# Kernel tuning notes

Hardware: AMD Instinct MI355X
Metric: run time of the kernel (lower is better)

Reference implementation:

```python
import jax, jax.numpy as jnp
import numpy as np

N_PARTS = 4
HIDDEN = 256
NUM_FREQS = 10
IN_DIM = 3
EMB_DIM = IN_DIM * (1 + 2 * NUM_FREQS)  # 63
PART_DIM = HIDDEN // N_PARTS


def _embed(x):
    freqs = 2.0 ** jnp.arange(NUM_FREQS, dtype=x.dtype)        # [F]
    xf = x[..., None, :] * freqs[:, None]                      # [..., F, 3]
    enc = jnp.stack([jnp.sin(xf), jnp.cos(xf)], axis=-2)       # [..., F, 2, 3]
    enc = enc.reshape(x.shape[:-1] + (NUM_FREQS * 2 * IN_DIM,))
    return jnp.concatenate([x, enc], axis=-1)                  # [..., 63]


def _masks():
    # contiguous 0/1 per-part neuron masks over the HIDDEN axis (ClassMaskCreator)
    m = np.zeros((N_PARTS, HIDDEN), dtype=np.float32)
    for p in range(N_PARTS):
        s = p * PART_DIM
        e = HIDDEN if p == N_PARTS - 1 else s + PART_DIM
        m[p, s:e] = 1.0
    return jnp.asarray(m)


def setup_inputs() -> dict:
    key = jax.random.key(0)
    ks = jax.random.split(key, 8)
    B, N = 1, 131072

    def lin(k, fan_in, fan_out):
        return jax.random.normal(k, (fan_in, fan_out), jnp.float32) / np.float32(np.sqrt(fan_in))

    return {
        "coords": jax.random.normal(ks[0], (B, N, IN_DIM), jnp.float32),
        "W0": lin(ks[1], EMB_DIM, HIDDEN), "b0": jnp.zeros((HIDDEN,), jnp.float32),
        "W1": lin(ks[2], HIDDEN, HIDDEN), "b1": jnp.zeros((HIDDEN,), jnp.float32),
        "W2": lin(ks[3], HIDDEN, HIDDEN), "b2": jnp.zeros((HIDDEN,), jnp.float32),
        "Wocc": lin(ks[4], HIDDEN, 1), "bocc": jnp.zeros((1,), jnp.float32),
        "Wc": jax.random.normal(ks[5], (N_PARTS, HIDDEN), jnp.float32) / np.float32(np.sqrt(HIDDEN)),
        "bc": jnp.zeros((N_PARTS,), jnp.float32),
    }


def reference(coords, W0, b0, W1, b1, W2, b2, Wocc, bocc, Wc, bc):
    masks = _masks()                                  # [P, H]
    x = _embed(coords) @ W0 + b0                      # [B, N, H]  (no activation after layer 0, per source)

    # occupancy trunk: relu(L1) -> relu(L2) -> occ head
    x_occ = jax.nn.relu(x @ W1 + b1)
    x_occ = jax.nn.relu(x_occ @ W2 + b2)
    occ = x_occ @ Wocc + bocc                         # [B, N, 1]

    # part branches. Loop iteration i=0 masks x; i=1 indexes temporal_part_output[1*part_id],
    # i.e. the i=0 outputs. The i=1 outputs (h2) are dead w.r.t. all returned values because
    # part_features[part_id] for part_id in 0..P-1 selects the first P (i=0) entries.
    h1 = [jax.nn.relu((x * masks[p]) @ W1 + b1) for p in range(N_PARTS)]  # [B, N, H] each

    # class heads: class_heads[p](h1[p] * mask_p).squeeze(0), concatenated on last dim
    cls = [jnp.squeeze((h1[p] * masks[p]) @ Wc[p][:, None] + bc[p], axis=0)
           for p in range(N_PARTS)]                   # [N, 1] each (B == 1)
    part_class = jnp.concatenate(cls, axis=-1)        # [N, P]

    return occ, part_class
```

## Files before the change

kernel.cpp:

```cpp
#include <hip/hip_runtime.h>


#define NPTS 131072
#define M_PB 64
#define AST 264

typedef _Float16 half8   __attribute__((ext_vector_type(8)));
typedef _Float16 half4_t __attribute__((ext_vector_type(4)));
typedef __fp16   fp16x2  __attribute__((ext_vector_type(2)));
typedef float    float4_t __attribute__((ext_vector_type(4)));

__global__ void prep(const float* __restrict__ W0, const float* __restrict__ W1,
                     const float* __restrict__ W2, _Float16* __restrict__ ws) {
  int id = blockIdx.x * 256 + threadIdx.x;
  _Float16 v;
  if (id < 16384) {
    int e = id, j = e & 7, l = (e >> 3) & 63, kb = (e >> 9) & 1, tt = e >> 10;
    int c = l & 15, q = l >> 4;
    int k = kb * 32 + q * 8 + j, n = tt * 16 + c;
    v = (k < 63) ? (_Float16)W0[k * 256 + n] : (_Float16)0.f;
  } else if (id < 81920) {
    int e = id - 16384, j = e & 7, l = (e >> 3) & 63, kb = (e >> 9) & 7, tt = e >> 12;
    int c = l & 15, q = l >> 4;
    int k = kb * 32 + q * 8 + j, n = tt * 16 + c;
    v = (_Float16)W1[k * 256 + n];
  } else {
    int e = id - 81920, j = e & 7, l = (e >> 3) & 63, kb = (e >> 9) & 7, tt = e >> 12;
    int c = l & 15, q = l >> 4;
    int k = kb * 32 + q * 8 + j, n = tt * 16 + c;
    v = (_Float16)W2[k * 256 + n];
  }
  ws[id] = v;
}

__device__ __forceinline__ half4_t pack4(float a, float b, float cc, float d) {
  fp16x2 p0 = __builtin_amdgcn_cvt_pkrtz(a, b);
  fp16x2 p1 = __builtin_amdgcn_cvt_pkrtz(cc, d);
  half4_t h;
  h[0] = (_Float16)p0[0]; h[1] = (_Float16)p0[1];
  h[2] = (_Float16)p1[0]; h[3] = (_Float16)p1[1];
  return h;
}

__global__ __launch_bounds__(256, 3) void mlp_main(
    const float* __restrict__ coords,
    const _Float16* __restrict__ W0sw,
    const _Float16* __restrict__ W1sw,
    const _Float16* __restrict__ W2sw,
    const float* __restrict__ b0, const float* __restrict__ b1,
    const float* __restrict__ b2,
    const float* __restrict__ Wocc, const float* __restrict__ bocc,
    const float* __restrict__ Wc, const float* __restrict__ bc,
    float* __restrict__ out) {
  __shared__ _Float16 actX[M_PB * AST];
  __shared__ float occ_s[4][M_PB];

  const int t = threadIdx.x;
  const int w = t >> 6;
  const int l = t & 63;
  const int c = l & 15;
  const int q = l >> 4;
  const int m0 = blockIdx.x * M_PB;

  {
    const float* cp = coords + (size_t)(m0 + l) * 3;
    float x0 = cp[0], x1 = cp[1], x2 = cp[2];
    float v[16];
#pragma unroll
    for (int u = 0; u < 16; ++u) {
      int k = 16 * w + u;
      float r;
      if (k >= 63) r = 0.f;
      else if (k < 3) r = (k == 0) ? x0 : (k == 1 ? x1 : x2);
      else {
        int kk = k - 3;
        int f = kk / 6;
        int rem = kk - 6 * f;
        int s = (rem >= 3) ? 1 : 0;
        int i3 = rem - 3 * s;
        float xi = (i3 == 0) ? x0 : (i3 == 1 ? x1 : x2);
        float arg = xi * (float)(1 << f);
        float nn = rintf(arg * 0.15915494309189535f);
        float rr = fmaf(nn, -6.28318548202514648f, arg);
        rr = fmaf(nn, 1.7484555e-7f, rr);
        r = s ? __cosf(rr) : __sinf(rr);
      }
      v[u] = r;
    }
    half8 e0, e1;
#pragma unroll
    for (int u = 0; u < 4; ++u) {
      fp16x2 p = __builtin_amdgcn_cvt_pkrtz(v[2 * u], v[2 * u + 1]);
      e0[2 * u] = (_Float16)p[0]; e0[2 * u + 1] = (_Float16)p[1];
      fp16x2 p2 = __builtin_amdgcn_cvt_pkrtz(v[8 + 2 * u], v[9 + 2 * u]);
      e1[2 * u] = (_Float16)p2[0]; e1[2 * u + 1] = (_Float16)p2[1];
    }
    *(half8*)&actX[l * AST + 16 * w] = e0;
    *(half8*)&actX[l * AST + 16 * w + 8] = e1;
  }
  __syncthreads();

  float4_t acc[4][4];
  const _Float16* ap = actX + c * AST + q * 8;

  {
    const _Float16* wb = W0sw + (size_t)(w * 4) * 1024 + l * 8;
    half8 a0[4], a1[4];
#pragma unroll
    for (int tn = 0; tn < 4; ++tn) {
      a0[tn] = *(const half8*)(wb + tn * 1024);
      a1[tn] = *(const half8*)(wb + tn * 1024 + 512);
    }
#pragma unroll
    for (int tn = 0; tn < 4; ++tn) {
      float4_t bz = *(const float4_t*)(b0 + 64 * w + tn * 16 + q * 4);
#pragma unroll
      for (int tm = 0; tm < 4; ++tm) acc[tn][tm] = bz;
    }
#pragma unroll
    for (int kb = 0; kb < 2; ++kb) {
      half8 b[4];
#pragma unroll
      for (int tm = 0; tm < 4; ++tm) b[tm] = *(const half8*)(ap + tm * 16 * AST + kb * 32);
#pragma unroll
      for (int tn = 0; tn < 4; ++tn)
#pragma unroll
        for (int tm = 0; tm < 4; ++tm)
          acc[tn][tm] = __builtin_amdgcn_mfma_f32_16x16x32_f16(
              kb ? a1[tn] : a0[tn], b[tm], acc[tn][tm], 0, 0, 0);
    }
  }
  __syncthreads();
#pragma unroll
  for (int tn = 0; tn < 4; ++tn)
#pragma unroll
    for (int tm = 0; tm < 4; ++tm) {
      float4_t v = acc[tn][tm];
      *(half4_t*)&actX[(tm * 16 + c) * AST + 64 * w + tn * 16 + q * 4] =
          pack4(v[0], v[1], v[2], v[3]);
    }
  __syncthreads();

  {
    const _Float16* wb = W1sw + (size_t)(w * 4) * 4096 + l * 8;
    const int w2 = 2 * w;
    float bcw = bc[w];
#pragma unroll
    for (int tn = 0; tn < 4; ++tn) {
      float4_t bz = *(const float4_t*)(b1 + 64 * w + tn * 16 + q * 4);
#pragma unroll
      for (int tm = 0; tm < 4; ++tm) acc[tn][tm] = bz;
    }
    auto kbof = [&](int j) {
      return (j < 2) ? (w2 + j) : ((j - 2) + ((j - 2) >= w2 ? 2 : 0));
    };
    half8 a[4], an[4];
#pragma unroll
    for (int tn = 0; tn < 4; ++tn) a[tn] = *(const half8*)(wb + tn * 4096 + kbof(0) * 512);
#pragma unroll
    for (int j = 0; j < 8; ++j) {
      const int kb = kbof(j);
      half8 b[4];
#pragma unroll
      for (int tm = 0; tm < 4; ++tm) b[tm] = *(const half8*)(ap + tm * 16 * AST + kb * 32);
      if (j + 1 < 8) {
        const int kbn = kbof(j + 1);
#pragma unroll
        for (int tn = 0; tn < 4; ++tn) an[tn] = *(const half8*)(wb + tn * 4096 + kbn * 512);
      }
#pragma unroll
      for (int tn = 0; tn < 4; ++tn)
#pragma unroll
        for (int tm = 0; tm < 4; ++tm)
          acc[tn][tm] = __builtin_amdgcn_mfma_f32_16x16x32_f16(a[tn], b[tm], acc[tn][tm], 0, 0, 0);
      if (j == 1) {
        float pcls[4] = {0.f, 0.f, 0.f, 0.f};
#pragma unroll
        for (int tn = 0; tn < 4; ++tn) {
          float4_t wcv = *(const float4_t*)(Wc + 256 * w + 64 * w + tn * 16 + q * 4);
#pragma unroll
          for (int tm = 0; tm < 4; ++tm) {
            float4_t v = acc[tn][tm];
#pragma unroll
            for (int r = 0; r < 4; ++r) pcls[tm] += fmaxf(v[r], 0.f) * wcv[r];
          }
        }
#pragma unroll
        for (int tm = 0; tm < 4; ++tm) {
          float s = pcls[tm];
          s += __shfl_xor(s, 16, 64);
          s += __shfl_xor(s, 32, 64);
          if (l < 16)
            out[(size_t)NPTS + (size_t)(m0 + tm * 16 + c) * 4 + w] = s + bcw;
        }
      }
      if (j + 1 < 8) {
#pragma unroll
        for (int tn = 0; tn < 4; ++tn) a[tn] = an[tn];
      }
    }
  }
  __syncthreads();
#pragma unroll
  for (int tn = 0; tn < 4; ++tn)
#pragma unroll
    for (int tm = 0; tm < 4; ++tm) {
      float4_t v = acc[tn][tm];
      *(half4_t*)&actX[(tm * 16 + c) * AST + 64 * w + tn * 16 + q * 4] =
          pack4(fmaxf(v[0], 0.f), fmaxf(v[1], 0.f), fmaxf(v[2], 0.f), fmaxf(v[3], 0.f));
    }
  __syncthreads();

  {
    const _Float16* wb = W2sw + (size_t)(w * 4) * 4096 + l * 8;
#pragma unroll
    for (int tn = 0; tn < 4; ++tn) {
      float4_t bz = *(const float4_t*)(b2 + 64 * w + tn * 16 + q * 4);
#pragma unroll
      for (int tm = 0; tm < 4; ++tm) acc[tn][tm] = bz;
    }
    half8 a[4], an[4];
#pragma unroll
    for (int tn = 0; tn < 4; ++tn) a[tn] = *(const half8*)(wb + tn * 4096);
#pragma unroll
    for (int kb = 0; kb < 8; ++kb) {
      half8 b[4];
#pragma unroll
      for (int tm = 0; tm < 4; ++tm) b[tm] = *(const half8*)(ap + tm * 16 * AST + kb * 32);
      if (kb + 1 < 8) {
#pragma unroll
        for (int tn = 0; tn < 4; ++tn)
          an[tn] = *(const half8*)(wb + tn * 4096 + (kb + 1) * 512);
      }
#pragma unroll
      for (int tn = 0; tn < 4; ++tn)
#pragma unroll
        for (int tm = 0; tm < 4; ++tm)
          acc[tn][tm] = __builtin_amdgcn_mfma_f32_16x16x32_f16(a[tn], b[tm], acc[tn][tm], 0, 0, 0);
      if (kb + 1 < 8) {
#pragma unroll
        for (int tn = 0; tn < 4; ++tn) a[tn] = an[tn];
      }
    }
    float pocc[4] = {0.f, 0.f, 0.f, 0.f};
#pragma unroll
    for (int tn = 0; tn < 4; ++tn) {
      float4_t wov = *(const float4_t*)(Wocc + 64 * w + tn * 16 + q * 4);
#pragma unroll
      for (int tm = 0; tm < 4; ++tm) {
        float4_t v = acc[tn][tm];
#pragma unroll
        for (int r = 0; r < 4; ++r) pocc[tm] += fmaxf(v[r], 0.f) * wov[r];
      }
    }
#pragma unroll
    for (int tm = 0; tm < 4; ++tm) {
      float s = pocc[tm];
      s += __shfl_xor(s, 16, 64);
      s += __shfl_xor(s, 32, 64);
      if (l < 16) occ_s[w][tm * 16 + c] = s;
    }
  }
  __syncthreads();
  if (t < M_PB) {
    out[m0 + t] = occ_s[0][t] + occ_s[1][t] + occ_s[2][t] + occ_s[3][t] + bocc[0];
  }
}

extern "C" void kernel_launch(void* const* d_in, const int* in_sizes, int n_in,
                              void* d_out, int out_size, void* d_ws, size_t ws_size,
                              hipStream_t stream) {
  const float* coords = (const float*)d_in[0];
  const float* W0   = (const float*)d_in[1];
  const float* b0   = (const float*)d_in[2];
  const float* W1   = (const float*)d_in[3];
  const float* b1   = (const float*)d_in[4];
  const float* W2   = (const float*)d_in[5];
  const float* b2   = (const float*)d_in[6];
  const float* Wocc = (const float*)d_in[7];
  const float* bocc = (const float*)d_in[8];
  const float* Wc   = (const float*)d_in[9];
  const float* bc   = (const float*)d_in[10];
  float* out = (float*)d_out;

  _Float16* ws = (_Float16*)d_ws;
  _Float16* W0sw = ws;
  _Float16* W1sw = ws + 16384;
  _Float16* W2sw = ws + 81920;

  prep<<<576, 256, 0, stream>>>(W0, W1, W2, ws);
  mlp_main<<<NPTS / M_PB, 256, 0, stream>>>(coords, W0sw, W1sw, W2sw,
                                            b0, b1, b2, Wocc, bocc, Wc, bc, out);
}
```

Before: 121.9 us.

## Double per-block point tile to 128 and deepen weight prefetch to three stages

Each block now handles 128 points instead of 64, so every wave runs a 4x8 grid of MFMA tiles and reuses each weight fragment across twice as many points, roughly halving weight traffic per point. The swizzled weight layout is reordered so that each wave's 64-column slice is contiguous per k-block. The one-stage weight prefetch becomes a rotating three-stage register buffer. The cost is double the accumulator registers and larger LDS use, with launch bounds lowered to 2 blocks per SM, so occupancy falls and register spills are possible.

```diff
diff --git a/kernel.cpp b/kernel.cpp
--- a/kernel.cpp
+++ b/kernel.cpp
@@ -2,7 +2,7 @@
 
 
 #define NPTS 131072
-#define M_PB 64
+#define M_PB 128
 #define AST 264
 
 typedef _Float16 half8   __attribute__((ext_vector_type(8)));
@@ -15,19 +15,16 @@
   int id = blockIdx.x * 256 + threadIdx.x;
   _Float16 v;
   if (id < 16384) {
-    int e = id, j = e & 7, l = (e >> 3) & 63, kb = (e >> 9) & 1, tt = e >> 10;
-    int c = l & 15, q = l >> 4;
-    int k = kb * 32 + q * 8 + j, n = tt * 16 + c;
+    int e = id, j = e & 7, l = (e >> 3) & 63, tn = (e >> 9) & 3, kb = (e >> 11) & 1, s = e >> 12;
+    int k = kb * 32 + (l >> 4) * 8 + j, n = s * 64 + tn * 16 + (l & 15);
     v = (k < 63) ? (_Float16)W0[k * 256 + n] : (_Float16)0.f;
   } else if (id < 81920) {
-    int e = id - 16384, j = e & 7, l = (e >> 3) & 63, kb = (e >> 9) & 7, tt = e >> 12;
-    int c = l & 15, q = l >> 4;
-    int k = kb * 32 + q * 8 + j, n = tt * 16 + c;
+    int e = id - 16384, j = e & 7, l = (e >> 3) & 63, tn = (e >> 9) & 3, kb = (e >> 11) & 7, s = e >> 14;
+    int k = kb * 32 + (l >> 4) * 8 + j, n = s * 64 + tn * 16 + (l & 15);
     v = (_Float16)W1[k * 256 + n];
   } else {
-    int e = id - 81920, j = e & 7, l = (e >> 3) & 63, kb = (e >> 9) & 7, tt = e >> 12;
-    int c = l & 15, q = l >> 4;
-    int k = kb * 32 + q * 8 + j, n = tt * 16 + c;
+    int e = id - 81920, j = e & 7, l = (e >> 3) & 63, tn = (e >> 9) & 3, kb = (e >> 11) & 7, s = e >> 14;
+    int k = kb * 32 + (l >> 4) * 8 + j, n = s * 64 + tn * 16 + (l & 15);
     v = (_Float16)W2[k * 256 + n];
   }
   ws[id] = v;
@@ -42,7 +39,7 @@
   return h;
 }
 
-__global__ __launch_bounds__(256, 3) void mlp_main(
+__global__ __launch_bounds__(256, 2) void mlp_main(
     const float* __restrict__ coords,
     const _Float16* __restrict__ W0sw,
     const _Float16* __restrict__ W1sw,
@@ -63,69 +60,70 @@
   const int m0 = blockIdx.x * M_PB;
 
   {
-    const float* cp = coords + (size_t)(m0 + l) * 3;
+    int m = t & 127, kh = (t >> 7) * 32;
+    const float* cp = coords + (size_t)(m0 + m) * 3;
     float x0 = cp[0], x1 = cp[1], x2 = cp[2];
-    float v[16];
-#pragma unroll
-    for (int u = 0; u < 16; ++u) {
-      int k = 16 * w + u;
-      float r;
-      if (k >= 63) r = 0.f;
-      else if (k < 3) r = (k == 0) ? x0 : (k == 1 ? x1 : x2);
-      else {
-        int kk = k - 3;
-        int f = kk / 6;
-        int rem = kk - 6 * f;
-        int s = (rem >= 3) ? 1 : 0;
-        int i3 = rem - 3 * s;
-        float xi = (i3 == 0) ? x0 : (i3 == 1 ? x1 : x2);
-        float arg = xi * (float)(1 << f);
-        float nn = rintf(arg * 0.15915494309189535f);
-        float rr = fmaf(nn, -6.28318548202514648f, arg);
-        rr = fmaf(nn, 1.7484555e-7f, rr);
-        r = s ? __cosf(rr) : __sinf(rr);
-      }
-      v[u] = r;
-    }
-    half8 e0, e1;
-#pragma unroll
-    for (int u = 0; u < 4; ++u) {
-      fp16x2 p = __builtin_amdgcn_cvt_pkrtz(v[2 * u], v[2 * u + 1]);
-      e0[2 * u] = (_Float16)p[0]; e0[2 * u + 1] = (_Float16)p[1];
-      fp16x2 p2 = __builtin_amdgcn_cvt_pkrtz(v[8 + 2 * u], v[9 + 2 * u]);
-      e1[2 * u] = (_Float16)p2[0]; e1[2 * u + 1] = (_Float16)p2[1];
-    }
-    *(half8*)&actX[l * AST + 16 * w] = e0;
-    *(half8*)&actX[l * AST + 16 * w + 8] = e1;
-  }
-  __syncthreads();
-
-  float4_t acc[4][4];
+#pragma unroll
+    for (int i = 0; i < 4; ++i) {
+      float v[8];
+#pragma unroll
+      for (int u = 0; u < 8; ++u) {
+        int k = kh + i * 8 + u;
+        float r;
+        if (k >= 63) r = 0.f;
+        else if (k < 3) r = (k == 0) ? x0 : (k == 1 ? x1 : x2);
+        else {
+          int kk = k - 3;
+          int f = kk / 6;
+          int rem = kk - 6 * f;
+          int s = (rem >= 3) ? 1 : 0;
+          int i3 = rem - 3 * s;
+          float xi = (i3 == 0) ? x0 : (i3 == 1 ? x1 : x2);
+          float arg = xi * (float)(1 << f);
+          float nn = rintf(arg * 0.15915494309189535f);
+          float rr = fmaf(nn, -6.28318548202514648f, arg);
+          rr = fmaf(nn, 1.7484555e-7f, rr);
+          r = s ? __cosf(rr) : __sinf(rr);
+        }
+        v[u] = r;
+      }
+      half8 ev;
+#pragma unroll
+      for (int u = 0; u < 4; ++u) {
+        fp16x2 p = __builtin_amdgcn_cvt_pkrtz(v[2 * u], v[2 * u + 1]);
+        ev[2 * u] = (_Float16)p[0]; ev[2 * u + 1] = (_Float16)p[1];
+      }
+      *(half8*)&actX[m * AST + kh + i * 8] = ev;
+    }
+  }
+  __syncthreads();
+
+  float4_t acc[4][8];
   const _Float16* ap = actX + c * AST + q * 8;
 
   {
-    const _Float16* wb = W0sw + (size_t)(w * 4) * 1024 + l * 8;
+    const _Float16* wb = W0sw + (size_t)w * 4096 + l * 8;
     half8 a0[4], a1[4];
 #pragma unroll
     for (int tn = 0; tn < 4; ++tn) {
-      a0[tn] = *(const half8*)(wb + tn * 1024);
-      a1[tn] = *(const half8*)(wb + tn * 1024 + 512);
+      a0[tn] = *(const half8*)(wb + tn * 512);
+      a1[tn] = *(const half8*)(wb + 2048 + tn * 512);
     }
 #pragma unroll
     for (int tn = 0; tn < 4; ++tn) {
       float4_t bz = *(const float4_t*)(b0 + 64 * w + tn * 16 + q * 4);
 #pragma unroll
-      for (int tm = 0; tm < 4; ++tm) acc[tn][tm] = bz;
+      for (int tm = 0; tm < 8; ++tm) acc[tn][tm] = bz;
     }
 #pragma unroll
     for (int kb = 0; kb < 2; ++kb) {
-      half8 b[4];
-#pragma unroll
-      for (int tm = 0; tm < 4; ++tm) b[tm] = *(const half8*)(ap + tm * 16 * AST + kb * 32);
-#pragma unroll
-      for (int tn = 0; tn < 4; ++tn)
-#pragma unroll
-        for (int tm = 0; tm < 4; ++tm)
+      half8 b[8];
+#pragma unroll
+      for (int tm = 0; tm < 8; ++tm) b[tm] = *(const half8*)(ap + tm * 16 * AST + kb * 32);
+#pragma unroll
+      for (int tn = 0; tn < 4; ++tn)
+#pragma unroll
+        for (int tm = 0; tm < 8; ++tm)
           acc[tn][tm] = __builtin_amdgcn_mfma_f32_16x16x32_f16(
               kb ? a1[tn] : a0[tn], b[tm], acc[tn][tm], 0, 0, 0);
     }
@@ -134,7 +132,7 @@
 #pragma unroll
   for (int tn = 0; tn < 4; ++tn)
 #pragma unroll
-    for (int tm = 0; tm < 4; ++tm) {
+    for (int tm = 0; tm < 8; ++tm) {
       float4_t v = acc[tn][tm];
       *(half4_t*)&actX[(tm * 16 + c) * AST + 64 * w + tn * 16 + q * 4] =
           pack4(v[0], v[1], v[2], v[3]);
@@ -142,51 +140,51 @@
   __syncthreads();
 
   {
-    const _Float16* wb = W1sw + (size_t)(w * 4) * 4096 + l * 8;
+    const _Float16* wb = W1sw + (size_t)w * 16384 + l * 8;
     const int w2 = 2 * w;
     float bcw = bc[w];
 #pragma unroll
     for (int tn = 0; tn < 4; ++tn) {
       float4_t bz = *(const float4_t*)(b1 + 64 * w + tn * 16 + q * 4);
 #pragma unroll
-      for (int tm = 0; tm < 4; ++tm) acc[tn][tm] = bz;
+      for (int tm = 0; tm < 8; ++tm) acc[tn][tm] = bz;
     }
     auto kbof = [&](int j) {
       return (j < 2) ? (w2 + j) : ((j - 2) + ((j - 2) >= w2 ? 2 : 0));
     };
-    half8 a[4], an[4];
-#pragma unroll
-    for (int tn = 0; tn < 4; ++tn) a[tn] = *(const half8*)(wb + tn * 4096 + kbof(0) * 512);
+    half8 A[3][4];
+#pragma unroll
+    for (int p = 0; p < 3; ++p) {
+      const _Float16* pa = wb + kbof(p) * 2048;
+#pragma unroll
+      for (int tn = 0; tn < 4; ++tn) A[p][tn] = *(const half8*)(pa + tn * 512);
+    }
 #pragma unroll
     for (int j = 0; j < 8; ++j) {
       const int kb = kbof(j);
-      half8 b[4];
-#pragma unroll
-      for (int tm = 0; tm < 4; ++tm) b[tm] = *(const half8*)(ap + tm * 16 * AST + kb * 32);
-      if (j + 1 < 8) {
-        const int kbn = kbof(j + 1);
-#pragma unroll
-        for (int tn = 0; tn < 4; ++tn) an[tn] = *(const half8*)(wb + tn * 4096 + kbn * 512);
-      }
-#pragma unroll
-      for (int tn = 0; tn < 4; ++tn)
-#pragma unroll
-        for (int tm = 0; tm < 4; ++tm)
-          acc[tn][tm] = __builtin_amdgcn_mfma_f32_16x16x32_f16(a[tn], b[tm], acc[tn][tm], 0, 0, 0);
+      half8 b[8];
+#pragma unroll
+      for (int tm = 0; tm < 8; ++tm) b[tm] = *(const half8*)(ap + tm * 16 * AST + kb * 32);
+#pragma unroll
+      for (int tn = 0; tn < 4; ++tn)
+#pragma unroll
+        for (int tm = 0; tm < 8; ++tm)
+          acc[tn][tm] = __builtin_amdgcn_mfma_f32_16x16x32_f16(
+              A[j % 3][tn], b[tm], acc[tn][tm], 0, 0, 0);
       if (j == 1) {
-        float pcls[4] = {0.f, 0.f, 0.f, 0.f};
+        float pcls[8] = {0.f, 0.f, 0.f, 0.f, 0.f, 0.f, 0.f, 0.f};
 #pragma unroll
         for (int tn = 0; tn < 4; ++tn) {
           float4_t wcv = *(const float4_t*)(Wc + 256 * w + 64 * w + tn * 16 + q * 4);
 #pragma unroll
-          for (int tm = 0; tm < 4; ++tm) {
+          for (int tm = 0; tm < 8; ++tm) {
             float4_t v = acc[tn][tm];
 #pragma unroll
             for (int r = 0; r < 4; ++r) pcls[tm] += fmaxf(v[r], 0.f) * wcv[r];
           }
         }
 #pragma unroll
-        for (int tm = 0; tm < 4; ++tm) {
+        for (int tm = 0; tm < 8; ++tm) {
           float s = pcls[tm];
           s += __shfl_xor(s, 16, 64);
           s += __shfl_xor(s, 32, 64);
@@ -194,9 +192,10 @@
             out[(size_t)NPTS + (size_t)(m0 + tm * 16 + c) * 4 + w] = s + bcw;
         }
       }
-      if (j + 1 < 8) {
-#pragma unroll
-        for (int tn = 0; tn < 4; ++tn) a[tn] = an[tn];
+      if (j + 3 < 8) {
+        const _Float16* pa = wb + kbof(j + 3) * 2048;
+#pragma unroll
+        for (int tn = 0; tn < 4; ++tn) A[j % 3][tn] = *(const half8*)(pa + tn * 512);
       }
     }
   }
@@ -204,7 +203,7 @@
 #pragma unroll
   for (int tn = 0; tn < 4; ++tn)
 #pragma unroll
-    for (int tm = 0; tm < 4; ++tm) {
+    for (int tm = 0; tm < 8; ++tm) {
       float4_t v = acc[tn][tm];
       *(half4_t*)&actX[(tm * 16 + c) * AST + 64 * w + tn * 16 + q * 4] =
           pack4(fmaxf(v[0], 0.f), fmaxf(v[1], 0.f), fmaxf(v[2], 0.f), fmaxf(v[3], 0.f));
@@ -212,49 +211,49 @@
   __syncthreads();
 
   {
-    const _Float16* wb = W2sw + (size_t)(w * 4) * 4096 + l * 8;
+    const _Float16* wb = W2sw + (size_t)w * 16384 + l * 8;
 #pragma unroll
     for (int tn = 0; tn < 4; ++tn) {
       float4_t bz = *(const float4_t*)(b2 + 64 * w + tn * 16 + q * 4);
 #pragma unroll
-      for (int tm = 0; tm < 4; ++tm) acc[tn][tm] = bz;
-    }
-    half8 a[4], an[4];
-#pragma unroll
-    for (int tn = 0; tn < 4; ++tn) a[tn] = *(const half8*)(wb + tn * 4096);
+      for (int tm = 0; tm < 8; ++tm) acc[tn][tm] = bz;
+    }
+    half8 A[3][4];
+#pragma unroll
+    for (int p = 0; p < 3; ++p)
+#pragma unroll
+      for (int tn = 0; tn < 4; ++tn)
+        A[p][tn] = *(const half8*)(wb + p * 2048 + tn * 512);
 #pragma unroll
     for (int kb = 0; kb < 8; ++kb) {
-      half8 b[4];
-#pragma unroll
-      for (int tm = 0; tm < 4; ++tm) b[tm] = *(const half8*)(ap + tm * 16 * AST + kb * 32);
-      if (kb + 1 < 8) {
+      half8 b[8];
+#pragma unroll
+      for (int tm = 0; tm < 8; ++tm) b[tm] = *(const half8*)(ap + tm * 16 * AST + kb * 32);
+#pragma unroll
+      for (int tn = 0; tn < 4; ++tn)
+#pragma unroll
+        for (int tm = 0; tm < 8; ++tm)
+          acc[tn][tm] = __builtin_amdgcn_mfma_f32_16x16x32_f16(
+              A[kb % 3][tn], b[tm], acc[tn][tm], 0, 0, 0);
+      if (kb + 3 < 8) {
 #pragma unroll
         for (int tn = 0; tn < 4; ++tn)
-          an[tn] = *(const half8*)(wb + tn * 4096 + (kb + 1) * 512);
-      }
-#pragma unroll
-      for (int tn = 0; tn < 4; ++tn)
-#pragma unroll
-        for (int tm = 0; tm < 4; ++tm)
-          acc[tn][tm] = __builtin_amdgcn_mfma_f32_16x16x32_f16(a[tn], b[tm], acc[tn][tm], 0, 0, 0);
-      if (kb + 1 < 8) {
-#pragma unroll
-        for (int tn = 0; tn < 4; ++tn) a[tn] = an[tn];
-      }
-    }
-    float pocc[4] = {0.f, 0.f, 0.f, 0.f};
+          A[kb % 3][tn] = *(const half8*)(wb + (kb + 3) * 2048 + tn * 512);
+      }
+    }
+    float pocc[8] = {0.f, 0.f, 0.f, 0.f, 0.f, 0.f, 0.f, 0.f};
 #pragma unroll
     for (int tn = 0; tn < 4; ++tn) {
       float4_t wov = *(const float4_t*)(Wocc + 64 * w + tn * 16 + q * 4);
 #pragma unroll
-      for (int tm = 0; tm < 4; ++tm) {
+      for (int tm = 0; tm < 8; ++tm) {
         float4_t v = acc[tn][tm];
 #pragma unroll
         for (int r = 0; r < 4; ++r) pocc[tm] += fmaxf(v[r], 0.f) * wov[r];
       }
     }
 #pragma unroll
-    for (int tm = 0; tm < 4; ++tm) {
+    for (int tm = 0; tm < 8; ++tm) {
       float s = pocc[tm];
       s += __shfl_xor(s, 16, 64);
       s += __shfl_xor(s, 32, 64);
```

Result: faster. 115.6 us (-5.1%).

## Reorder swizzled weights per wave and double-buffer global weight prefetch across layers

Applied to the files above, without the earlier changes.

Changes the prep swizzle so each wave's weight fragments for a k-block sit contiguously, and writes the embedding into a separate small LDS buffer so layer-0 no longer needs a barrier before reusing actX. Weight fragments are now prefetched two k-blocks ahead and across layer boundaries (next layer's first fragments load while the current epilogue runs), and LDS activation reads are software-pipelined one step ahead. The aim is to hide global-memory weight latency and remove one syncthreads, at the cost of more registers and extra LDS, which could lower occupancy under the 3-block launch bound.

```diff
diff --git a/kernel.cpp b/kernel.cpp
--- a/kernel.cpp
+++ b/kernel.cpp
@@ -4,6 +4,7 @@
 #define NPTS 131072
 #define M_PB 64
 #define AST 264
+#define EST 72
 
 typedef _Float16 half8   __attribute__((ext_vector_type(8)));
 typedef _Float16 half4_t __attribute__((ext_vector_type(4)));
@@ -15,19 +16,16 @@
   int id = blockIdx.x * 256 + threadIdx.x;
   _Float16 v;
   if (id < 16384) {
-    int e = id, j = e & 7, l = (e >> 3) & 63, kb = (e >> 9) & 1, tt = e >> 10;
-    int c = l & 15, q = l >> 4;
-    int k = kb * 32 + q * 8 + j, n = tt * 16 + c;
+    int e = id, j = e & 7, l = (e >> 3) & 63, tn = (e >> 9) & 3, kb = (e >> 11) & 1, s = e >> 12;
+    int k = kb * 32 + (l >> 4) * 8 + j, n = s * 64 + tn * 16 + (l & 15);
     v = (k < 63) ? (_Float16)W0[k * 256 + n] : (_Float16)0.f;
   } else if (id < 81920) {
-    int e = id - 16384, j = e & 7, l = (e >> 3) & 63, kb = (e >> 9) & 7, tt = e >> 12;
-    int c = l & 15, q = l >> 4;
-    int k = kb * 32 + q * 8 + j, n = tt * 16 + c;
+    int e = id - 16384, j = e & 7, l = (e >> 3) & 63, tn = (e >> 9) & 3, kb = (e >> 11) & 7, s = e >> 14;
+    int k = kb * 32 + (l >> 4) * 8 + j, n = s * 64 + tn * 16 + (l & 15);
     v = (_Float16)W1[k * 256 + n];
   } else {
-    int e = id - 81920, j = e & 7, l = (e >> 3) & 63, kb = (e >> 9) & 7, tt = e >> 12;
-    int c = l & 15, q = l >> 4;
-    int k = kb * 32 + q * 8 + j, n = tt * 16 + c;
+    int e = id - 81920, j = e & 7, l = (e >> 3) & 63, tn = (e >> 9) & 3, kb = (e >> 11) & 7, s = e >> 14;
+    int k = kb * 32 + (l >> 4) * 8 + j, n = s * 64 + tn * 16 + (l & 15);
     v = (_Float16)W2[k * 256 + n];
   }
   ws[id] = v;
@@ -52,6 +50,7 @@
     const float* __restrict__ Wocc, const float* __restrict__ bocc,
     const float* __restrict__ Wc, const float* __restrict__ bc,
     float* __restrict__ out) {
+  __shared__ _Float16 ebuf[M_PB * EST];
   __shared__ _Float16 actX[M_PB * AST];
   __shared__ float occ_s[4][M_PB];
 
@@ -95,22 +94,37 @@
       fp16x2 p2 = __builtin_amdgcn_cvt_pkrtz(v[8 + 2 * u], v[9 + 2 * u]);
       e1[2 * u] = (_Float16)p2[0]; e1[2 * u + 1] = (_Float16)p2[1];
     }
-    *(half8*)&actX[l * AST + 16 * w] = e0;
-    *(half8*)&actX[l * AST + 16 * w + 8] = e1;
+    *(half8*)&ebuf[l * EST + 16 * w] = e0;
+    *(half8*)&ebuf[l * EST + 16 * w + 8] = e1;
+  }
+
+  half8 A[2][4];
+  {
+    const _Float16* wb = W0sw + (size_t)w * 4096 + l * 8;
+#pragma unroll
+    for (int tn = 0; tn < 4; ++tn) {
+      A[0][tn] = *(const half8*)(wb + tn * 512);
+      A[1][tn] = *(const half8*)(wb + 2048 + tn * 512);
+    }
   }
   __syncthreads();
 
   float4_t acc[4][4];
   const _Float16* ap = actX + c * AST + q * 8;
-
-  {
-    const _Float16* wb = W0sw + (size_t)(w * 4) * 1024 + l * 8;
-    half8 a0[4], a1[4];
-#pragma unroll
-    for (int tn = 0; tn < 4; ++tn) {
-      a0[tn] = *(const half8*)(wb + tn * 1024);
-      a1[tn] = *(const half8*)(wb + tn * 1024 + 512);
-    }
+  const _Float16* ep = ebuf + c * EST + q * 8;
+  const int w2 = 2 * w;
+  auto kbof = [&](int j) {
+    return (j < 2) ? (w2 + j) : ((j - 2) + ((j - 2) >= w2 ? 2 : 0));
+  };
+  const _Float16* wb1 = W1sw + (size_t)w * 16384 + l * 8;
+  const _Float16* wb2 = W2sw + (size_t)w * 16384 + l * 8;
+
+  {
+    half8 bc0[4], bc1[4];
+#pragma unroll
+    for (int tm = 0; tm < 4; ++tm) bc0[tm] = *(const half8*)(ep + tm * 16 * EST);
+#pragma unroll
+    for (int tm = 0; tm < 4; ++tm) bc1[tm] = *(const half8*)(ep + tm * 16 * EST + 32);
 #pragma unroll
     for (int tn = 0; tn < 4; ++tn) {
       float4_t bz = *(const float4_t*)(b0 + 64 * w + tn * 16 + q * 4);
@@ -118,19 +132,22 @@
       for (int tm = 0; tm < 4; ++tm) acc[tn][tm] = bz;
     }
 #pragma unroll
-    for (int kb = 0; kb < 2; ++kb) {
-      half8 b[4];
-#pragma unroll
-      for (int tm = 0; tm < 4; ++tm) b[tm] = *(const half8*)(ap + tm * 16 * AST + kb * 32);
-#pragma unroll
-      for (int tn = 0; tn < 4; ++tn)
-#pragma unroll
-        for (int tm = 0; tm < 4; ++tm)
-          acc[tn][tm] = __builtin_amdgcn_mfma_f32_16x16x32_f16(
-              kb ? a1[tn] : a0[tn], b[tm], acc[tn][tm], 0, 0, 0);
-    }
-  }
-  __syncthreads();
+    for (int tn = 0; tn < 4; ++tn)
+#pragma unroll
+      for (int tm = 0; tm < 4; ++tm)
+        acc[tn][tm] = __builtin_amdgcn_mfma_f32_16x16x32_f16(A[0][tn], bc0[tm], acc[tn][tm], 0, 0, 0);
+#pragma unroll
+    for (int tn = 0; tn < 4; ++tn)
+#pragma unroll
+      for (int tm = 0; tm < 4; ++tm)
+        acc[tn][tm] = __builtin_amdgcn_mfma_f32_16x16x32_f16(A[1][tn], bc1[tm], acc[tn][tm], 0, 0, 0);
+  }
+#pragma unroll
+  for (int p = 0; p < 2; ++p) {
+    const _Float16* pa = wb1 + kbof(p) * 2048;
+#pragma unroll
+    for (int tn = 0; tn < 4; ++tn) A[p][tn] = *(const half8*)(pa + tn * 512);
+  }
 #pragma unroll
   for (int tn = 0; tn < 4; ++tn)
 #pragma unroll
@@ -142,8 +159,6 @@
   __syncthreads();
 
   {
-    const _Float16* wb = W1sw + (size_t)(w * 4) * 4096 + l * 8;
-    const int w2 = 2 * w;
     float bcw = bc[w];
 #pragma unroll
     for (int tn = 0; tn < 4; ++tn) {
@@ -151,28 +166,25 @@
 #pragma unroll
       for (int tm = 0; tm < 4; ++tm) acc[tn][tm] = bz;
     }
-    auto kbof = [&](int j) {
-      return (j < 2) ? (w2 + j) : ((j - 2) + ((j - 2) >= w2 ? 2 : 0));
-    };
-    half8 a[4], an[4];
-#pragma unroll
-    for (int tn = 0; tn < 4; ++tn) a[tn] = *(const half8*)(wb + tn * 4096 + kbof(0) * 512);
+    half8 bcur[4];
+#pragma unroll
+    for (int tm = 0; tm < 4; ++tm)
+      bcur[tm] = *(const half8*)(ap + tm * 16 * AST + kbof(0) * 32);
 #pragma unroll
     for (int j = 0; j < 8; ++j) {
-      const int kb = kbof(j);
-      half8 b[4];
-#pragma unroll
-      for (int tm = 0; tm < 4; ++tm) b[tm] = *(const half8*)(ap + tm * 16 * AST + kb * 32);
+      half8 bnxt[4];
       if (j + 1 < 8) {
         const int kbn = kbof(j + 1);
 #pragma unroll
-        for (int tn = 0; tn < 4; ++tn) an[tn] = *(const half8*)(wb + tn * 4096 + kbn * 512);
+        for (int tm = 0; tm < 4; ++tm)
+          bnxt[tm] = *(const half8*)(ap + tm * 16 * AST + kbn * 32);
       }
 #pragma unroll
       for (int tn = 0; tn < 4; ++tn)
 #pragma unroll
         for (int tm = 0; tm < 4; ++tm)
-          acc[tn][tm] = __builtin_amdgcn_mfma_f32_16x16x32_f16(a[tn], b[tm], acc[tn][tm], 0, 0, 0);
+          acc[tn][tm] = __builtin_amdgcn_mfma_f32_16x16x32_f16(
+              A[j & 1][tn], bcur[tm], acc[tn][tm], 0, 0, 0);
       if (j == 1) {
         float pcls[4] = {0.f, 0.f, 0.f, 0.f};
 #pragma unroll
@@ -194,12 +206,20 @@
             out[(size_t)NPTS + (size_t)(m0 + tm * 16 + c) * 4 + w] = s + bcw;
         }
       }
-      if (j + 1 < 8) {
-#pragma unroll
-        for (int tn = 0; tn < 4; ++tn) a[tn] = an[tn];
-      }
-    }
-  }
+      if (j + 2 < 8) {
+        const _Float16* pa = wb1 + kbof(j + 2) * 2048;
+#pragma unroll
+        for (int tn = 0; tn < 4; ++tn) A[j & 1][tn] = *(const half8*)(pa + tn * 512);
+      }
+#pragma unroll
+      for (int tm = 0; tm < 4; ++tm) bcur[tm] = bnxt[tm];
+    }
+  }
+#pragma unroll
+  for (int p = 0; p < 2; ++p)
+#pragma unroll
+    for (int tn = 0; tn < 4; ++tn)
+      A[p][tn] = *(const half8*)(wb2 + p * 2048 + tn * 512);
   __syncthreads();
 #pragma unroll
   for (int tn = 0; tn < 4; ++tn)
@@ -212,35 +232,36 @@
   __syncthreads();
 
   {
-    const _Float16* wb = W2sw + (size_t)(w * 4) * 4096 + l * 8;
 #pragma unroll
     for (int tn = 0; tn < 4; ++tn) {
       float4_t bz = *(const float4_t*)(b2 + 64 * w + tn * 16 + q * 4);
 #pragma unroll
       for (int tm = 0; tm < 4; ++tm) acc[tn][tm] = bz;
     }
-    half8 a[4], an[4];
-#pragma unroll
-    for (int tn = 0; tn < 4; ++tn) a[tn] = *(const half8*)(wb + tn * 4096);
+    half8 bcur[4];
+#pragma unroll
+    for (int tm = 0; tm < 4; ++tm) bcur[tm] = *(const half8*)(ap + tm * 16 * AST);
 #pragma unroll
     for (int kb = 0; kb < 8; ++kb) {
-      half8 b[4];
-#pragma unroll
-      for (int tm = 0; tm < 4; ++tm) b[tm] = *(const half8*)(ap + tm * 16 * AST + kb * 32);
+      half8 bnxt[4];
       if (kb + 1 < 8) {
 #pragma unroll
+        for (int tm = 0; tm < 4; ++tm)
+          bnxt[tm] = *(const half8*)(ap + tm * 16 * AST + (kb + 1) * 32);
+      }
+#pragma unroll
+      for (int tn = 0; tn < 4; ++tn)
+#pragma unroll
+        for (int tm = 0; tm < 4; ++tm)
+          acc[tn][tm] = __builtin_amdgcn_mfma_f32_16x16x32_f16(
+              A[kb & 1][tn], bcur[tm], acc[tn][tm], 0, 0, 0);
+      if (kb + 2 < 8) {
+#pragma unroll
         for (int tn = 0; tn < 4; ++tn)
-          an[tn] = *(const half8*)(wb + tn * 4096 + (kb + 1) * 512);
-      }
-#pragma unroll
-      for (int tn = 0; tn < 4; ++tn)
-#pragma unroll
-        for (int tm = 0; tm < 4; ++tm)
-          acc[tn][tm] = __builtin_amdgcn_mfma_f32_16x16x32_f16(a[tn], b[tm], acc[tn][tm], 0, 0, 0);
-      if (kb + 1 < 8) {
-#pragma unroll
-        for (int tn = 0; tn < 4; ++tn) a[tn] = an[tn];
-      }
+          A[kb & 1][tn] = *(const half8*)(wb2 + (kb + 2) * 2048 + tn * 512);
+      }
+#pragma unroll
+      for (int tm = 0; tm < 4; ++tm) bcur[tm] = bnxt[tm];
     }
     float pocc[4] = {0.f, 0.f, 0.f, 0.f};
 #pragma unroll
```

Measured after the change: 118.8 us. 2.5% less time.
